# Optimization experiments

Hardware: AMD Instinct MI355X
Metric: run time of the kernel (lower is better)

The kernel has to match this reference:

```python
import jax, jax.numpy as jnp
import numpy as np

NUM_GROUPS = 32
EPS = 1e-5


def setup_inputs() -> dict:
    key = jax.random.key(0)
    k1, k2 = jax.random.split(key)
    N, C = 1000000, 128
    num_instances = 100
    features = jax.random.normal(k1, (N, C), dtype=jnp.float32)
    ins_indices_batch = jax.random.randint(k2, (N,), 0, num_instances, dtype=jnp.int64)
    gamma = jnp.ones((C,), dtype=jnp.float32)
    beta = jnp.zeros((C,), dtype=jnp.float32)
    return {
        "features": features,
        "ins_indices_batch": ins_indices_batch,
        "gamma": gamma,
        "beta": beta,
        "num_instances": num_instances,
    }


def reference(features, ins_indices_batch, gamma, beta, num_instances):
    # Segmented GroupNorm: for each instance id i, the original gathers rows
    # where ins_indices_batch == i into a [1, C, L] tensor and applies
    # nn.GroupNorm(G, C): stats over (C//G channels x L positions) per group.
    N, C = features.shape
    G = NUM_GROUPS
    Cg = C // G
    seg = ins_indices_batch.astype(jnp.int32)

    # Per-(segment, channel) sums -> per-(segment, group) stats. Single pass.
    sums = jax.ops.segment_sum(features, seg, num_segments=num_instances)        # [S, C]
    sqs = jax.ops.segment_sum(features * features, seg, num_segments=num_instances)  # [S, C]
    cnt = jax.ops.segment_sum(jnp.ones((N,), features.dtype), seg, num_segments=num_instances)  # [S]

    gsum = sums.reshape(num_instances, G, Cg).sum(axis=-1)   # [S, G]
    gsq = sqs.reshape(num_instances, G, Cg).sum(axis=-1)     # [S, G]
    denom = jnp.maximum(cnt[:, None] * Cg, 1.0)               # [S, G]
    mean = gsum / denom
    var = gsq / denom - mean * mean                            # biased var (GroupNorm)
    inv = jax.lax.rsqrt(var + EPS)                             # [S, G]

    # Scatter stats back to each row and normalize (fused elementwise).
    mean_n = mean[seg]  # [N, G]
    inv_n = inv[seg]    # [N, G]
    xg = features.reshape(N, G, Cg)
    xn = (xg - mean_n[:, :, None]) * inv_n[:, :, None]
    out = xn.reshape(N, C) * gamma + beta
    return out
```

## Files before the change

kernel.cpp:

```cpp
#include <hip/hip_runtime.h>


#define C_CHANNELS 128
#define GROUPS 32
#define SEG_CAP 256
#define LDS_SEG_CAP 104
#define EPS 1e-5f

typedef float f32x4 __attribute__((ext_vector_type(4)));

__device__ __forceinline__ void lds_fadd(float* p, float v) {
    asm volatile("ds_add_f32 %0, %1"
                 :: "v"((unsigned)(unsigned long long)p), "v"(v));
}

__device__ __forceinline__ void nt_store4(float4* p, const float4& v) {
    f32x4 t; t.x = v.x; t.y = v.y; t.z = v.z; t.w = v.w;
    __builtin_nontemporal_store(t, (f32x4*)p);
}

__global__ __launch_bounds__(256) void gn_pass1(
    const float4* __restrict__ x, const int* __restrict__ seg,
    float* __restrict__ gsum, float* __restrict__ gsq, float* __restrict__ gcnt,
    const int* __restrict__ nInstPtr, int N)
{
    __shared__ float lsum[LDS_SEG_CAP * GROUPS];
    __shared__ float lsq [LDS_SEG_CAP * GROUPS];
    __shared__ float lcnt[LDS_SEG_CAP];

    for (int t = threadIdx.x; t < LDS_SEG_CAP * GROUPS; t += blockDim.x) {
        lsum[t] = 0.f; lsq[t] = 0.f;
    }
    for (int t = threadIdx.x; t < LDS_SEG_CAP; t += blockDim.x) lcnt[t] = 0.f;
    __syncthreads();

    const int g = threadIdx.x & 31;
    const long long total  = (long long)N * GROUPS;
    const long long stride = (long long)gridDim.x * blockDim.x;
    const int rowStride = (int)(stride >> 5);
    long long i = (long long)blockIdx.x * blockDim.x + threadIdx.x;

    for (; i + 3 * stride < total; i += 4 * stride) {
        int row0 = (int)(i >> 5);
        float4 v0 = x[i];
        float4 v1 = x[i + stride];
        float4 v2 = x[i + 2 * stride];
        float4 v3 = x[i + 3 * stride];
        int s0 = seg[row0];
        int s1 = seg[row0 + rowStride];
        int s2 = seg[row0 + 2 * rowStride];
        int s3 = seg[row0 + 3 * rowStride];

        float a0 = (v0.x + v0.y) + (v0.z + v0.w);
        float q0 = v0.x*v0.x + v0.y*v0.y + v0.z*v0.z + v0.w*v0.w;
        float a1 = (v1.x + v1.y) + (v1.z + v1.w);
        float q1 = v1.x*v1.x + v1.y*v1.y + v1.z*v1.z + v1.w*v1.w;
        float a2 = (v2.x + v2.y) + (v2.z + v2.w);
        float q2 = v2.x*v2.x + v2.y*v2.y + v2.z*v2.z + v2.w*v2.w;
        float a3 = (v3.x + v3.y) + (v3.z + v3.w);
        float q3 = v3.x*v3.x + v3.y*v3.y + v3.z*v3.z + v3.w*v3.w;

        if (s0 < LDS_SEG_CAP) {
            lds_fadd(&lsum[s0 * GROUPS + g], a0);
            lds_fadd(&lsq [s0 * GROUPS + g], q0);
            if (g == 0) lds_fadd(&lcnt[s0], 1.0f);
        } else {
            unsafeAtomicAdd(&gsum[s0 * GROUPS + g], a0);
            unsafeAtomicAdd(&gsq [s0 * GROUPS + g], q0);
            if (g == 0) unsafeAtomicAdd(&gcnt[s0], 1.0f);
        }
        if (s1 < LDS_SEG_CAP) {
            lds_fadd(&lsum[s1 * GROUPS + g], a1);
            lds_fadd(&lsq [s1 * GROUPS + g], q1);
            if (g == 0) lds_fadd(&lcnt[s1], 1.0f);
        } else {
            unsafeAtomicAdd(&gsum[s1 * GROUPS + g], a1);
            unsafeAtomicAdd(&gsq [s1 * GROUPS + g], q1);
            if (g == 0) unsafeAtomicAdd(&gcnt[s1], 1.0f);
        }
        if (s2 < LDS_SEG_CAP) {
            lds_fadd(&lsum[s2 * GROUPS + g], a2);
            lds_fadd(&lsq [s2 * GROUPS + g], q2);
            if (g == 0) lds_fadd(&lcnt[s2], 1.0f);
        } else {
            unsafeAtomicAdd(&gsum[s2 * GROUPS + g], a2);
            unsafeAtomicAdd(&gsq [s2 * GROUPS + g], q2);
            if (g == 0) unsafeAtomicAdd(&gcnt[s2], 1.0f);
        }
        if (s3 < LDS_SEG_CAP) {
            lds_fadd(&lsum[s3 * GROUPS + g], a3);
            lds_fadd(&lsq [s3 * GROUPS + g], q3);
            if (g == 0) lds_fadd(&lcnt[s3], 1.0f);
        } else {
            unsafeAtomicAdd(&gsum[s3 * GROUPS + g], a3);
            unsafeAtomicAdd(&gsq [s3 * GROUPS + g], q3);
            if (g == 0) unsafeAtomicAdd(&gcnt[s3], 1.0f);
        }
    }
    for (; i < total; i += stride) {
        int row = (int)(i >> 5);
        float4 v = x[i];
        int s = seg[row];
        float a = (v.x + v.y) + (v.z + v.w);
        float q = v.x*v.x + v.y*v.y + v.z*v.z + v.w*v.w;
        if (s < LDS_SEG_CAP) {
            lds_fadd(&lsum[s * GROUPS + g], a);
            lds_fadd(&lsq [s * GROUPS + g], q);
            if (g == 0) lds_fadd(&lcnt[s], 1.0f);
        } else {
            unsafeAtomicAdd(&gsum[s * GROUPS + g], a);
            unsafeAtomicAdd(&gsq [s * GROUPS + g], q);
            if (g == 0) unsafeAtomicAdd(&gcnt[s], 1.0f);
        }
    }

    asm volatile("s_waitcnt lgkmcnt(0)" ::: "memory");
    __syncthreads();

    int S = *nInstPtr;
    int lim = min(S, LDS_SEG_CAP);
    int nb = lim * GROUPS;
    int rot = (int)((blockIdx.x * 64u) % (unsigned)nb);
    for (int t = threadIdx.x; t < nb; t += blockDim.x) {
        int j = t + rot; if (j >= nb) j -= nb;
        float a = lsum[j], b = lsq[j];
        if (a != 0.f || b != 0.f) {
            unsafeAtomicAdd(&gsum[j], a);
            unsafeAtomicAdd(&gsq [j], b);
        }
    }
    for (int t = threadIdx.x; t < lim; t += blockDim.x) {
        float c = lcnt[t];
        if (c != 0.f) unsafeAtomicAdd(&gcnt[t], c);
    }
}

__global__ __launch_bounds__(256) void gn_finalize(
    const float* __restrict__ gsum, const float* __restrict__ gsq,
    const float* __restrict__ gcnt, float2* __restrict__ stats,
    const int* __restrict__ nInstPtr)
{
    int S = *nInstPtr;
    int i = blockIdx.x * blockDim.x + threadIdx.x;
    if (i < S * GROUPS) {
        int s = i >> 5;
        float cnt = gcnt[s];
        float denom = fmaxf(cnt * 4.0f, 1.0f);
        float mean = gsum[i] / denom;
        float var  = gsq[i] / denom - mean * mean;
        float inv  = rsqrtf(var + EPS);
        stats[i] = make_float2(mean, inv);
    }
}

__global__ __launch_bounds__(256) void gn_pass2(
    const float4* __restrict__ x, const int* __restrict__ seg,
    const float2* __restrict__ stats,
    const float4* __restrict__ gamma4, const float4* __restrict__ beta4,
    float4* __restrict__ out, const int* __restrict__ nInstPtr, int N)
{
    __shared__ float lmean[LDS_SEG_CAP * GROUPS];
    __shared__ float linv [LDS_SEG_CAP * GROUPS];
    int S = *nInstPtr;
    int lim = min(S, LDS_SEG_CAP) * GROUPS;
    for (int t = threadIdx.x; t < lim; t += blockDim.x) {
        float2 mi = stats[t];
        lmean[t] = mi.x; linv[t] = mi.y;
    }
    __syncthreads();

    const int g = threadIdx.x & 31;
    const float4 gm = gamma4[g];
    const float4 bt = beta4[g];
    const long long total  = (long long)N * GROUPS;
    const long long stride = (long long)gridDim.x * blockDim.x;
    const int rowStride = (int)(stride >> 5);
    long long i = (long long)blockIdx.x * blockDim.x + threadIdx.x;

    for (; i + stride < total; i += 2 * stride) {
        int row0 = (int)(i >> 5);
        float4 v0 = x[i];
        float4 v1 = x[i + stride];
        int s0 = seg[row0];
        int s1 = seg[row0 + rowStride];

        float m0, iv0, m1, iv1;
        if (s0 < LDS_SEG_CAP) { m0 = lmean[s0 * GROUPS + g]; iv0 = linv[s0 * GROUPS + g]; }
        else { float2 t = stats[s0 * GROUPS + g]; m0 = t.x; iv0 = t.y; }
        if (s1 < LDS_SEG_CAP) { m1 = lmean[s1 * GROUPS + g]; iv1 = linv[s1 * GROUPS + g]; }
        else { float2 t = stats[s1 * GROUPS + g]; m1 = t.x; iv1 = t.y; }

        float4 o0, o1;
        o0.x = (v0.x - m0) * iv0 * gm.x + bt.x;
        o0.y = (v0.y - m0) * iv0 * gm.y + bt.y;
        o0.z = (v0.z - m0) * iv0 * gm.z + bt.z;
        o0.w = (v0.w - m0) * iv0 * gm.w + bt.w;
        o1.x = (v1.x - m1) * iv1 * gm.x + bt.x;
        o1.y = (v1.y - m1) * iv1 * gm.y + bt.y;
        o1.z = (v1.z - m1) * iv1 * gm.z + bt.z;
        o1.w = (v1.w - m1) * iv1 * gm.w + bt.w;

        nt_store4(&out[i], o0);
        nt_store4(&out[i + stride], o1);
    }
    for (; i < total; i += stride) {
        int row = (int)(i >> 5);
        float4 v = x[i];
        int s = seg[row];
        float m, iv;
        if (s < LDS_SEG_CAP) { m = lmean[s * GROUPS + g]; iv = linv[s * GROUPS + g]; }
        else { float2 t = stats[s * GROUPS + g]; m = t.x; iv = t.y; }
        float4 o;
        o.x = (v.x - m) * iv * gm.x + bt.x;
        o.y = (v.y - m) * iv * gm.y + bt.y;
        o.z = (v.z - m) * iv * gm.z + bt.z;
        o.w = (v.w - m) * iv * gm.w + bt.w;
        nt_store4(&out[i], o);
    }
}

extern "C" void kernel_launch(void* const* d_in, const int* in_sizes, int n_in,
                              void* d_out, int out_size, void* d_ws, size_t ws_size,
                              hipStream_t stream) {
    const float* feat  = (const float*)d_in[0];
    const int*   seg   = (const int*)d_in[1];
    const float* gamma = (const float*)d_in[2];
    const float* beta  = (const float*)d_in[3];
    const int*   nInst = (const int*)d_in[4];
    const int N = in_sizes[0] / C_CHANNELS;

    float* gsum = (float*)d_ws;
    float* gsq  = gsum + SEG_CAP * GROUPS;
    float* gcnt = gsq  + SEG_CAP * GROUPS;
    float2* stats = (float2*)(gcnt + SEG_CAP);
    size_t zero_bytes = (size_t)(2 * SEG_CAP * GROUPS + SEG_CAP) * sizeof(float);

    (void)hipMemsetAsync(d_ws, 0, zero_bytes, stream);

    gn_pass1<<<1536, 256, 0, stream>>>(
        (const float4*)feat, seg, gsum, gsq, gcnt, nInst, N);

    gn_finalize<<<(SEG_CAP * GROUPS + 255) / 256, 256, 0, stream>>>(
        gsum, gsq, gcnt, stats, nInst);

    gn_pass2<<<1536, 256, 0, stream>>>(
        (const float4*)feat, seg, stats,
        (const float4*)gamma, (const float4*)beta,
        (float4*)d_out, nInst, N);
}
```

Baseline: 1.119 ms.

## Replace atomic pass-1 reduction with counting-sort by segment then segmented reduce

```diff
diff --git a/kernel.cpp b/kernel.cpp
--- a/kernel.cpp
+++ b/kernel.cpp
@@ -9,14 +9,114 @@
 
 typedef float f32x4 __attribute__((ext_vector_type(4)));
 
+__device__ __forceinline__ void nt_store4(float4* p, const float4& v) {
+    f32x4 t; t.x = v.x; t.y = v.y; t.z = v.z; t.w = v.w;
+    __builtin_nontemporal_store(t, (f32x4*)p);
+}
+
+__global__ __launch_bounds__(256) void gn_hist(
+    const int* __restrict__ seg, unsigned* __restrict__ histU, int N)
+{
+    __shared__ unsigned h[SEG_CAP];
+    for (int t = threadIdx.x; t < SEG_CAP; t += blockDim.x) h[t] = 0u;
+    __syncthreads();
+    int stride = gridDim.x * blockDim.x;
+    for (int r = blockIdx.x * blockDim.x + threadIdx.x; r < N; r += stride) {
+        int s = seg[r];
+        if ((unsigned)s < SEG_CAP) atomicAdd(&h[s], 1u);
+    }
+    __syncthreads();
+    for (int t = threadIdx.x; t < SEG_CAP; t += blockDim.x) {
+        unsigned c = h[t];
+        if (c) atomicAdd(&histU[t], c);
+    }
+}
+
+__global__ __launch_bounds__(64) void gn_prefix(
+    const unsigned* __restrict__ histU, unsigned* __restrict__ boundsU,
+    unsigned* __restrict__ cursorU, float* __restrict__ gcntf,
+    const int* __restrict__ nInstPtr)
+{
+    if (threadIdx.x == 0 && blockIdx.x == 0) {
+        int S = *nInstPtr;
+        if (S > SEG_CAP) S = SEG_CAP;
+        unsigned run = 0;
+        for (int s = 0; s < S; ++s) {
+            unsigned c = histU[s];
+            boundsU[s] = run;
+            cursorU[s] = run;
+            gcntf[s]   = (float)c;
+            run += c;
+        }
+        boundsU[S] = run;
+    }
+}
+
+__global__ __launch_bounds__(256) void gn_scatter(
+    const int* __restrict__ seg, unsigned* __restrict__ cursorU,
+    unsigned* __restrict__ rowidx, int N)
+{
+    int stride = gridDim.x * blockDim.x;
+    for (int r = blockIdx.x * blockDim.x + threadIdx.x; r < N; r += stride) {
+        int s = seg[r];
+        if ((unsigned)s < SEG_CAP) {
+            unsigned pos = atomicAdd(&cursorU[s], 1u);
+            rowidx[pos] = (unsigned)r;
+        }
+    }
+}
+
+__global__ __launch_bounds__(256) void gn_reduce(
+    const float4* __restrict__ x, const unsigned* __restrict__ rowidx,
+    const unsigned* __restrict__ boundsU,
+    float* __restrict__ gsum, float* __restrict__ gsq,
+    const int* __restrict__ nInstPtr, int N)
+{
+    __shared__ int sb[SEG_CAP + 1];
+    int S = *nInstPtr;
+    if (S > SEG_CAP) S = SEG_CAP;
+    for (int t = threadIdx.x; t <= S; t += blockDim.x) sb[t] = (int)boundsU[t];
+    __syncthreads();
+
+    const int h = threadIdx.x >> 5;
+    const int g = threadIdx.x & 31;
+    int chunk = (N + gridDim.x - 1) / gridDim.x;
+    int start = blockIdx.x * chunk;
+    int end   = min(N, start + chunk);
+    int p = start + h;
+    if (p >= end) return;
+
+    int lo = 0, hi = S - 1;
+    while (lo < hi) {
+        int mid = (lo + hi) >> 1;
+        if (sb[mid + 1] <= p) lo = mid + 1; else hi = mid;
+    }
+    int k = lo;
+
+    float asum = 0.f, asq = 0.f;
+    for (; p < end; p += 8) {
+        while (p >= sb[k + 1]) {
+            if (asum != 0.f || asq != 0.f) {
+                unsafeAtomicAdd(&gsum[k * GROUPS + g], asum);
+                unsafeAtomicAdd(&gsq [k * GROUPS + g], asq);
+                asum = 0.f; asq = 0.f;
+            }
+            ++k;
+        }
+        int r = (int)rowidx[p];
+        float4 v = x[(long long)r * GROUPS + g];
+        asum += (v.x + v.y) + (v.z + v.w);
+        asq  += v.x*v.x + v.y*v.y + v.z*v.z + v.w*v.w;
+    }
+    if (asum != 0.f || asq != 0.f) {
+        unsafeAtomicAdd(&gsum[k * GROUPS + g], asum);
+        unsafeAtomicAdd(&gsq [k * GROUPS + g], asq);
+    }
+}
+
 __device__ __forceinline__ void lds_fadd(float* p, float v) {
     asm volatile("ds_add_f32 %0, %1"
                  :: "v"((unsigned)(unsigned long long)p), "v"(v));
-}
-
-__device__ __forceinline__ void nt_store4(float4* p, const float4& v) {
-    f32x4 t; t.x = v.x; t.y = v.y; t.z = v.z; t.w = v.w;
-    __builtin_nontemporal_store(t, (f32x4*)p);
 }
 
 __global__ __launch_bounds__(256) void gn_pass1(
@@ -37,66 +137,7 @@
     const int g = threadIdx.x & 31;
     const long long total  = (long long)N * GROUPS;
     const long long stride = (long long)gridDim.x * blockDim.x;
-    const int rowStride = (int)(stride >> 5);
     long long i = (long long)blockIdx.x * blockDim.x + threadIdx.x;
-
-    for (; i + 3 * stride < total; i += 4 * stride) {
-        int row0 = (int)(i >> 5);
-        float4 v0 = x[i];
-        float4 v1 = x[i + stride];
-        float4 v2 = x[i + 2 * stride];
-        float4 v3 = x[i + 3 * stride];
-        int s0 = seg[row0];
-        int s1 = seg[row0 + rowStride];
-        int s2 = seg[row0 + 2 * rowStride];
-        int s3 = seg[row0 + 3 * rowStride];
-
-        float a0 = (v0.x + v0.y) + (v0.z + v0.w);
-        float q0 = v0.x*v0.x + v0.y*v0.y + v0.z*v0.z + v0.w*v0.w;
-        float a1 = (v1.x + v1.y) + (v1.z + v1.w);
-        float q1 = v1.x*v1.x + v1.y*v1.y + v1.z*v1.z + v1.w*v1.w;
-        float a2 = (v2.x + v2.y) + (v2.z + v2.w);
-        float q2 = v2.x*v2.x + v2.y*v2.y + v2.z*v2.z + v2.w*v2.w;
-        float a3 = (v3.x + v3.y) + (v3.z + v3.w);
-        float q3 = v3.x*v3.x + v3.y*v3.y + v3.z*v3.z + v3.w*v3.w;
-
-        if (s0 < LDS_SEG_CAP) {
-            lds_fadd(&lsum[s0 * GROUPS + g], a0);
-            lds_fadd(&lsq [s0 * GROUPS + g], q0);
-            if (g == 0) lds_fadd(&lcnt[s0], 1.0f);
-        } else {
-            unsafeAtomicAdd(&gsum[s0 * GROUPS + g], a0);
-            unsafeAtomicAdd(&gsq [s0 * GROUPS + g], q0);
-            if (g == 0) unsafeAtomicAdd(&gcnt[s0], 1.0f);
-        }
-        if (s1 < LDS_SEG_CAP) {
-            lds_fadd(&lsum[s1 * GROUPS + g], a1);
-            lds_fadd(&lsq [s1 * GROUPS + g], q1);
-            if (g == 0) lds_fadd(&lcnt[s1], 1.0f);
-        } else {
-            unsafeAtomicAdd(&gsum[s1 * GROUPS + g], a1);
-            unsafeAtomicAdd(&gsq [s1 * GROUPS + g], q1);
-            if (g == 0) unsafeAtomicAdd(&gcnt[s1], 1.0f);
-        }
-        if (s2 < LDS_SEG_CAP) {
-            lds_fadd(&lsum[s2 * GROUPS + g], a2);
-            lds_fadd(&lsq [s2 * GROUPS + g], q2);
-            if (g == 0) lds_fadd(&lcnt[s2], 1.0f);
-        } else {
-            unsafeAtomicAdd(&gsum[s2 * GROUPS + g], a2);
-            unsafeAtomicAdd(&gsq [s2 * GROUPS + g], q2);
-            if (g == 0) unsafeAtomicAdd(&gcnt[s2], 1.0f);
-        }
-        if (s3 < LDS_SEG_CAP) {
-            lds_fadd(&lsum[s3 * GROUPS + g], a3);
-            lds_fadd(&lsq [s3 * GROUPS + g], q3);
-            if (g == 0) lds_fadd(&lcnt[s3], 1.0f);
-        } else {
-            unsafeAtomicAdd(&gsum[s3 * GROUPS + g], a3);
-            unsafeAtomicAdd(&gsq [s3 * GROUPS + g], q3);
-            if (g == 0) unsafeAtomicAdd(&gcnt[s3], 1.0f);
-        }
-    }
     for (; i < total; i += stride) {
         int row = (int)(i >> 5);
         float4 v = x[i];
@@ -113,7 +154,6 @@
             if (g == 0) unsafeAtomicAdd(&gcnt[s], 1.0f);
         }
     }
-
     asm volatile("s_waitcnt lgkmcnt(0)" ::: "memory");
     __syncthreads();
 
@@ -229,19 +269,36 @@
     const int*   nInst = (const int*)d_in[4];
     const int N = in_sizes[0] / C_CHANNELS;
 
-    float* gsum = (float*)d_ws;
-    float* gsq  = gsum + SEG_CAP * GROUPS;
-    float* gcnt = gsq  + SEG_CAP * GROUPS;
-    float2* stats = (float2*)(gcnt + SEG_CAP);
-    size_t zero_bytes = (size_t)(2 * SEG_CAP * GROUPS + SEG_CAP) * sizeof(float);
-
-    (void)hipMemsetAsync(d_ws, 0, zero_bytes, stream);
-
-    gn_pass1<<<1536, 256, 0, stream>>>(
-        (const float4*)feat, seg, gsum, gsq, gcnt, nInst, N);
-
-    gn_finalize<<<(SEG_CAP * GROUPS + 255) / 256, 256, 0, stream>>>(
-        gsum, gsq, gcnt, stats, nInst);
+    float*    base    = (float*)d_ws;
+    float*    gsum    = base;
+    float*    gsq     = base + 8192;
+    unsigned* histU   = (unsigned*)(base + 16384);
+    float*    gcntf   = base + 16640;
+    unsigned* cursorU = (unsigned*)(base + 16896);
+    unsigned* boundsU = (unsigned*)(base + 17152);
+    float2*   stats   = (float2*)(base + 17412);
+    unsigned* rowidx  = (unsigned*)(base + 33796);
+
+    size_t need = (size_t)33796 * 4 + (size_t)N * 4;
+    bool use_sorted = (ws_size >= need);
+
+    if (use_sorted) {
+        (void)hipMemsetAsync(d_ws, 0, (size_t)(16384 + 256) * 4, stream);
+
+        gn_hist<<<512, 256, 0, stream>>>(seg, histU, N);
+        gn_prefix<<<1, 64, 0, stream>>>(histU, boundsU, cursorU, gcntf, nInst);
+        gn_scatter<<<512, 256, 0, stream>>>(seg, cursorU, rowidx, N);
+        gn_reduce<<<2048, 256, 0, stream>>>(
+            (const float4*)feat, rowidx, boundsU, gsum, gsq, nInst, N);
+        gn_finalize<<<(SEG_CAP * GROUPS + 255) / 256, 256, 0, stream>>>(
+            gsum, gsq, gcntf, stats, nInst);
+    } else {
+        (void)hipMemsetAsync(d_ws, 0, (size_t)(16384 + 512) * 4, stream);
+        gn_pass1<<<1536, 256, 0, stream>>>(
+            (const float4*)feat, seg, gsum, gsq, gcntf, nInst, N);
+        gn_finalize<<<(SEG_CAP * GROUPS + 255) / 256, 256, 0, stream>>>(
+            gsum, gsq, gcntf, stats, nInst);
+    }
 
     gn_pass2<<<1536, 256, 0, stream>>>(
         (const float4*)feat, seg, stats,
```

Result: slower. 1.968 ms (+75.9%).
